# Performance work log

Measured on AMD Instinct MI355X. Metric: run time of the kernel, lower is better.

## Reference

```python
import jax, jax.numpy as jnp
import numpy as np
import math

HIDDEN = 128   # hidden_size (per-head dim) used for 1/sqrt(d) scaling
SPAN = 1024    # attn_span
B, M = 32, 1024
K_LEN = M + SPAN


def _unskew(X, span):
    """X: [B, M, K] -> [B, M, span], out[b,m,l] = X[b, m, m+l].
    Equivalent to the torch pad/view/slice trick (shift row m left by m)."""
    _, Mq, _ = X.shape
    rows = jnp.arange(Mq)[:, None]                 # [M,1]
    cols = rows + jnp.arange(span)[None, :]        # [M,span]
    return X[:, rows, cols]


def _skew(X, pad_value):
    """X: [B, M, L] -> [B, M, M+L], out[b,m,j] = X[b,m,j-m] if 0<=j-m<L else pad.
    Equivalent to the torch pad/view/slice trick (shift row m right by m)."""
    _, Mq, L = X.shape
    m = jnp.arange(Mq)[:, None]                    # [M,1]
    rel = jnp.arange(Mq + L)[None, :] - m          # [M, M+L]
    valid = (rel >= 0) & (rel < L)
    gathered = X[:, m, jnp.clip(rel, 0, L - 1)]    # [B, M, M+L]
    return jnp.where(valid, gathered, pad_value)


def setup_inputs() -> dict:
    key = jax.random.key(0)
    k1, k2, k3, k4 = jax.random.split(key, 4)
    return {
        "query": jax.random.normal(k1, (B, M, HIDDEN), dtype=jnp.float32),
        "key": jax.random.normal(k2, (B, K_LEN, HIDDEN), dtype=jnp.float32),
        "value": jax.random.normal(k3, (B, K_LEN, HIDDEN), dtype=jnp.float32),
        "pos_encoding": jax.random.normal(k4, (HIDDEN, SPAN), dtype=jnp.float32),
    }


def reference(query, key, value, pos_encoding):
    span = pos_encoding.shape[-1]
    # context scores: [B, M, M+span]
    attn_ctx = jnp.einsum('bmh,bkh->bmk', query, key)
    attn_ctx = _unskew(attn_ctx, span)             # [B, M, span]
    # relative-position scores: [B, M, span]
    attn_pos = jnp.einsum('bmh,hl->bml', query, pos_encoding)
    attn = (attn_ctx + attn_pos) / math.sqrt(HIDDEN)
    attn = jax.nn.softmax(attn, axis=-1)           # dropout p=0 -> identity
    attn_sk = _skew(attn, 0.0)                     # [B, M, M+span]
    return jnp.einsum('bmk,bkh->bmh', attn_sk, value)
```

## Files before the change

### kernel.cpp

```cpp
#include <hip/hip_runtime.h>
#include <hip/hip_bf16.h>

#define B_    32
#define M_    1024
#define H_    128
#define SPAN_ 1024
#define KL_   2048
#define NITER 17
#define SCALE 0.08838834764831845f

typedef __attribute__((ext_vector_type(8))) short bf16x8;
typedef __attribute__((ext_vector_type(4))) float f32x4;

#define QOFF 0ull
#define KOFF 8388608ull
#define VOFF 25165824ull
#define POFF 41943040ull
#define WSNEED 42205184ull

static __device__ __forceinline__ unsigned int cvt_pk2(float lo, float hi) {
  unsigned int r;
  asm("v_cvt_pk_bf16_f32 %0, %1, %2" : "=v"(r) : "v"(lo), "v"(hi));
  return r;
}
static __device__ __forceinline__ unsigned short f2b(float x) {
  unsigned int u = __builtin_bit_cast(unsigned int, x);
  return (unsigned short)((u + 0x7FFFu + ((u >> 16) & 1u)) >> 16);
}
static __device__ __forceinline__ float b2f(unsigned short u) {
  return __builtin_bit_cast(float, ((unsigned int)u) << 16);
}
static __device__ __forceinline__ bf16x8 ldfrag(const char* p) {
  short4 a = *(const short4*)p;
  short4 b = *(const short4*)(p + 8);
  bf16x8 r;
  r[0] = a.x; r[1] = a.y; r[2] = a.z; r[3] = a.w;
  r[4] = b.x; r[5] = b.y; r[6] = b.z; r[7] = b.w;
  return r;
}
static __device__ __forceinline__ void gll16(char* lds, const char* g) {
  __builtin_amdgcn_global_load_lds(
      (const __attribute__((address_space(1))) unsigned int*)g,
      (__attribute__((address_space(3))) unsigned int*)lds, 16, 0, 0);
}

__global__ void convA(const float* __restrict__ in, char* __restrict__ out,
                      int nunits, float scale) {
  int idx = blockIdx.x * 256 + threadIdx.x;
  if (idx >= nunits) return;
  int r = idx >> 4, u = idx & 15;
  const float* p = in + (size_t)r * 128 + u * 8;
  float4 a = *(const float4*)p, b = *(const float4*)(p + 4);
  uint4 d;
  d.x = cvt_pk2(a.x * scale, a.y * scale);
  d.y = cvt_pk2(a.z * scale, a.w * scale);
  d.z = cvt_pk2(b.x * scale, b.y * scale);
  d.w = cvt_pk2(b.z * scale, b.w * scale);
  *(uint4*)(out + (size_t)r * 256 + 16 * (u ^ (r & 7))) = d;
}

__global__ void convV(const float* __restrict__ v, char* __restrict__ out) {
  __shared__ float tile[64][130];
  int tb = blockIdx.x;
  const float* src = v + (size_t)tb * 64 * 128;
  int tid = threadIdx.x;
#pragma unroll
  for (int i = 0; i < 8; ++i) {
    int idx = i * 256 + tid;
    int row = idx >> 5, c4 = idx & 31;
    float4 x = *(const float4*)(src + row * 128 + c4 * 4);
    tile[row][c4 * 4 + 0] = x.x; tile[row][c4 * 4 + 1] = x.y;
    tile[row][c4 * 4 + 2] = x.z; tile[row][c4 * 4 + 3] = x.w;
  }
  __syncthreads();
  char* dst = out + (size_t)tb * 16384;
#pragma unroll
  for (int j = 0; j < 4; ++j) {
    int idx = j * 256 + tid;
    int h = idx >> 3, u = idx & 7;
    uint4 d;
    d.x = cvt_pk2(tile[8 * u + 0][h], tile[8 * u + 1][h]);
    d.y = cvt_pk2(tile[8 * u + 2][h], tile[8 * u + 3][h]);
    d.z = cvt_pk2(tile[8 * u + 4][h], tile[8 * u + 5][h]);
    d.w = cvt_pk2(tile[8 * u + 6][h], tile[8 * u + 7][h]);
    *(uint4*)(dst + h * 128 + 16 * (u ^ (h & 7))) = d;
  }
}

__global__ void convP(const float* __restrict__ pe, char* __restrict__ out) {
  __shared__ float tile[128][66];
  int lt = blockIdx.x, tid = threadIdx.x;
#pragma unroll
  for (int i = 0; i < 8; ++i) {
    int idx = i * 256 + tid;
    int h = idx >> 4, c4 = idx & 15;
    float4 x = *(const float4*)(pe + (size_t)h * 1024 + lt * 64 + c4 * 4);
    tile[h][c4 * 4 + 0] = x.x; tile[h][c4 * 4 + 1] = x.y;
    tile[h][c4 * 4 + 2] = x.z; tile[h][c4 * 4 + 3] = x.w;
  }
  __syncthreads();
  char* dst = out + (size_t)lt * 16384;
#pragma unroll
  for (int j = 0; j < 4; ++j) {
    int idx = j * 256 + tid;
    int l = idx >> 4, u = idx & 15;
    uint4 d;
    d.x = cvt_pk2(tile[8 * u + 0][l], tile[8 * u + 1][l]);
    d.y = cvt_pk2(tile[8 * u + 2][l], tile[8 * u + 3][l]);
    d.z = cvt_pk2(tile[8 * u + 4][l], tile[8 * u + 5][l]);
    d.w = cvt_pk2(tile[8 * u + 6][l], tile[8 * u + 7][l]);
    *(uint4*)(dst + l * 256 + 16 * (u ^ (l & 7))) = d;
  }
}

#define L_KL 0
#define L_VT 16384
#define L_PT 32768
#define L_PR 49152
#define L_PW 66048
#define LDS_MAIN 74752

__global__ void __launch_bounds__(256, 2) seqattn_main(
    const char* __restrict__ qws, const char* __restrict__ kws,
    const char* __restrict__ vws, const char* __restrict__ pws,
    float* __restrict__ out) {
  extern __shared__ char smem[];
  char* KL = smem + L_KL;
  char* VT = smem + L_VT;
  char* PT = smem + L_PT;
  char* PR = smem + L_PR;
  char* PW = smem + L_PW;

  int jb = blockIdx.x;
  int o  = (jb & 7) * 64 + (jb >> 3);
  int b  = o >> 4;
  int m0t = o & 15;

  int tid = threadIdx.x, w = tid >> 6, lane = tid & 63, g = lane >> 4, c = lane & 15;
  int mrow = 16 * w + c;
  int sx = c & 7;
  int foffA[4], foffV[2];
#pragma unroll
  for (int hs = 0; hs < 4; ++hs) foffA[hs] = 16 * (((hs << 2) | g) ^ sx);
  foffV[0] = 16 * (g ^ sx);
  foffV[1] = 16 * ((4 | g) ^ sx);

  const char* qsrc = qws + ((size_t)(b * 16 + m0t)) * 16384;
  const char* ksrc = kws + ((size_t)(b * 32 + m0t)) * 16384;
  const char* vsrc = vws + ((size_t)(b * 32 + m0t)) * 16384;

#pragma unroll
  for (int i = 0; i < 4; ++i)
    gll16(KL + (4 * w + i) * 1024, qsrc + (4 * w + i) * 1024 + lane * 16);
  __syncthreads();
  bf16x8 qf[4];
#pragma unroll
  for (int hs = 0; hs < 4; ++hs)
    qf[hs] = *(const bf16x8*)(KL + mrow * 256 + foffA[hs]);
  __syncthreads();
#pragma unroll
  for (int i = 0; i < 4; ++i) {
    gll16(KL + (4 * w + i) * 1024, ksrc + (4 * w + i) * 1024 + lane * 16);
    gll16(VT + (4 * w + i) * 1024, vsrc + (4 * w + i) * 1024 + lane * 16);
    gll16(PT + (4 * w + i) * 1024, pws + (4 * w + i) * 1024 + lane * 16);
  }
  __syncthreads();

  f32x4 O[8];
#pragma unroll
  for (int i = 0; i < 8; ++i) { O[i][0] = 0.f; O[i][1] = 0.f; O[i][2] = 0.f; O[i][3] = 0.f; }
  float mrun = -1e30f, lrun = 0.f;
  char* prRow = PR + mrow * 264;
  char* pwRow = PW + mrow * 136;

#pragma unroll 1
  for (int t = 0; t < NITER; ++t) {
    if (t < 16) {
#pragma unroll
      for (int lt = 0; lt < 4; ++lt) {
        f32x4 pb = {0.f, 0.f, 0.f, 0.f};
#pragma unroll
        for (int hs = 0; hs < 4; ++hs)
          pb = __builtin_amdgcn_mfma_f32_16x16x32_bf16(
              *(const bf16x8*)(PT + (16 * lt + c) * 256 + foffA[hs]), qf[hs], pb, 0, 0, 0);
#pragma unroll
        for (int rr = 0; rr < 4; ++rr) {
          int x = (64 * t + 16 * lt + 4 * g + rr + mrow) & 127;
          *(unsigned short*)(prRow + x * 2) = f2b(pb[rr]);
        }
      }
    }
    f32x4 s[4];
#pragma unroll
    for (int nt = 0; nt < 4; ++nt) {
      f32x4 acc = {0.f, 0.f, 0.f, 0.f};
#pragma unroll
      for (int hs = 0; hs < 4; ++hs)
        acc = __builtin_amdgcn_mfma_f32_16x16x32_bf16(
            *(const bf16x8*)(KL + (16 * nt + c) * 256 + foffA[hs]), qf[hs], acc, 0, 0, 0);
      s[nt] = acc;
    }
    bf16x8 vf[16];
#pragma unroll
    for (int nt = 0; nt < 8; ++nt)
#pragma unroll
      for (int ks = 0; ks < 2; ++ks)
        vf[nt * 2 + ks] = *(const bf16x8*)(VT + (16 * nt + c) * 128 + foffV[ks]);

    __syncthreads();
    if (t < 16) {
      const char* ks_ = ksrc + (size_t)(t + 1) * 16384;
      const char* vs_ = vsrc + (size_t)(t + 1) * 16384;
#pragma unroll
      for (int i = 0; i < 4; ++i) {
        gll16(KL + (4 * w + i) * 1024, ks_ + (4 * w + i) * 1024 + lane * 16);
        gll16(VT + (4 * w + i) * 1024, vs_ + (4 * w + i) * 1024 + lane * 16);
      }
      if (t < 15) {
        const char* ps_ = pws + (size_t)(t + 1) * 16384;
#pragma unroll
        for (int i = 0; i < 4; ++i)
          gll16(PT + (4 * w + i) * 1024, ps_ + (4 * w + i) * 1024 + lane * 16);
      }
    }

#pragma unroll
    for (int nt = 0; nt < 4; ++nt) {
      int x = (64 * t + 16 * nt + 4 * g) & 127;
      ushort4 bv = *(const ushort4*)(prRow + x * 2);
      int lbase = 64 * t + 16 * nt + 4 * g - mrow;
      const unsigned short* bp = (const unsigned short*)&bv;
#pragma unroll
      for (int rr = 0; rr < 4; ++rr) {
        float sv = s[nt][rr] + b2f(bp[rr]);
        s[nt][rr] = ((unsigned)(lbase + rr) < 1024u) ? sv : -1e30f;
      }
    }
    float pmax = -1e30f;
#pragma unroll
    for (int nt = 0; nt < 4; ++nt)
#pragma unroll
      for (int rr = 0; rr < 4; ++rr) pmax = fmaxf(pmax, s[nt][rr]);
    pmax = fmaxf(pmax, __shfl_xor(pmax, 16, 64));
    pmax = fmaxf(pmax, __shfl_xor(pmax, 32, 64));
    if (__any(pmax > mrun + 8.0f)) {
      float mn = fmaxf(mrun, pmax);
      float corr = __expf(mrun - mn);
      mrun = mn;
      lrun *= corr;
#pragma unroll
      for (int i = 0; i < 8; ++i) {
        O[i][0] *= corr; O[i][1] *= corr; O[i][2] *= corr; O[i][3] *= corr;
      }
    }
    float rsum = 0.f;
#pragma unroll
    for (int nt = 0; nt < 4; ++nt) {
      float p0 = __expf(s[nt][0] - mrun);
      float p1 = __expf(s[nt][1] - mrun);
      float p2 = __expf(s[nt][2] - mrun);
      float p3 = __expf(s[nt][3] - mrun);
      rsum += (p0 + p1) + (p2 + p3);
      uint2 d_;
      d_.x = cvt_pk2(p0, p1);
      d_.y = cvt_pk2(p2, p3);
      *(uint2*)(pwRow + (16 * nt + 4 * g) * 2) = d_;
    }
    rsum += __shfl_xor(rsum, 16, 64);
    rsum += __shfl_xor(rsum, 32, 64);
    lrun += rsum;
#pragma unroll
    for (int ks = 0; ks < 2; ++ks) {
      bf16x8 pfrag = ldfrag(pwRow + ks * 64 + g * 16);
#pragma unroll
      for (int nt = 0; nt < 8; ++nt)
        O[nt] = __builtin_amdgcn_mfma_f32_16x16x32_bf16(
            vf[nt * 2 + ks], pfrag, O[nt], 0, 0, 0);
    }
    __syncthreads();
  }

  float inv = 1.0f / lrun;
  float* ob = out + ((size_t)b * M_ + m0t * 64 + mrow) * H_;
#pragma unroll
  for (int nt = 0; nt < 8; ++nt) {
    float4 vv;
    vv.x = O[nt][0] * inv; vv.y = O[nt][1] * inv;
    vv.z = O[nt][2] * inv; vv.w = O[nt][3] * inv;
    *(float4*)(ob + 16 * nt + 4 * g) = vv;
  }
}

#define PITCH_A  264
#define PITCH_VT 136
#define PITCH_PR 264
#define PITCH_PW 136
#define OFF_K  0
#define OFF_VT 16896
#define OFF_PT 34304
#define OFF_PR 51200
#define OFF_PW 68096
#define LDS_FB 76800

__global__ void __launch_bounds__(256, 2) seqattn_fb(
    const float* __restrict__ q, const float* __restrict__ kkey,
    const float* __restrict__ vval, const float* __restrict__ pe,
    float* __restrict__ out) {
  extern __shared__ char smem[];
  char* KL = smem + OFF_K;
  char* VT = smem + OFF_VT;
  char* PT = smem + OFF_PT;
  char* PR = smem + OFF_PR;
  char* PW = smem + OFF_PW;

  int jb = blockIdx.x;
  int o  = (jb & 7) * 64 + (jb >> 3);
  int b  = o >> 4;
  int m0 = (o & 15) * 64;

  int tid  = threadIdx.x;
  int w    = tid >> 6;
  int lane = tid & 63;
  int g    = lane >> 4;
  int c    = lane & 15;
  int r0   = tid >> 5;
  int c4   = tid & 31;

  const float* qbase = q    + ((size_t)b * M_  + m0) * H_;
  const float* kbase = kkey + ((size_t)b * KL_ + m0) * H_;
  const float* vbase = vval + ((size_t)b * KL_ + m0) * H_;

  float4 kpre[8];
  float  vpre[32];
  float  ppre[32];

#define LOADK(tt) do {                                                        \
    const float* kb_ = kbase + (size_t)(64 * (tt)) * H_;                      \
    _Pragma("unroll")                                                         \
    for (int p = 0; p < 8; ++p)                                               \
      kpre[p] = *(const float4*)(kb_ + (p * 8 + r0) * H_ + c4 * 4);           \
  } while (0)
#define WRITEK() do {                                                         \
    _Pragma("unroll")                                                         \
    for (int p = 0; p < 8; ++p) {                                             \
      float4 v_ = kpre[p];                                                    \
      uint2 d_; d_.x = cvt_pk2(v_.x, v_.y); d_.y = cvt_pk2(v_.z, v_.w);       \
      *(uint2*)(KL + (p * 8 + r0) * PITCH_A + c4 * 8) = d_;                   \
    }                                                                         \
  } while (0)
#define LOADV(tt) do {                                                        \
    const float* vb_ = vbase + (size_t)(64 * (tt)) * H_;                      \
    _Pragma("unroll")                                                         \
    for (int qq = 0; qq < 4; ++qq) {                                          \
      int kq_ = 4 * (4 * w + qq);                                             \
      _Pragma("unroll")                                                       \
      for (int r = 0; r < 4; ++r) {                                           \
        vpre[qq * 8 + r * 2 + 0] = vb_[(kq_ + r) * H_ + lane];                \
        vpre[qq * 8 + r * 2 + 1] = vb_[(kq_ + r) * H_ + lane + 64];           \
      }                                                                       \
    }                                                                         \
  } while (0)
#define WRITEV() do {                                                         \
    _Pragma("unroll")                                                         \
    for (int qq = 0; qq < 4; ++qq) {                                          \
      int kq_ = 4 * w + qq;                                                   \
      uint2 lo_, hi_;                                                         \
      lo_.x = cvt_pk2(vpre[qq * 8 + 0], vpre[qq * 8 + 2]);                    \
      lo_.y = cvt_pk2(vpre[qq * 8 + 4], vpre[qq * 8 + 6]);                    \
      hi_.x = cvt_pk2(vpre[qq * 8 + 1], vpre[qq * 8 + 3]);                    \
      hi_.y = cvt_pk2(vpre[qq * 8 + 5], vpre[qq * 8 + 7]);                    \
      *(uint2*)(VT + lane * PITCH_VT + 8 * kq_) = lo_;                        \
      *(uint2*)(VT + (lane + 64) * PITCH_VT + 8 * kq_) = hi_;                 \
    }                                                                         \
  } while (0)
#define LOADP(tt) do {                                                        \
    const float* pb_ = pe + 64 * (tt);                                        \
    _Pragma("unroll")                                                         \
    for (int qq = 0; qq < 8; ++qq) {                                          \
      int h_ = 4 * (8 * w + qq);                                              \
      _Pragma("unroll")                                                       \
      for (int r = 0; r < 4; ++r)                                             \
        ppre[qq * 4 + r] = pb_[(h_ + r) * SPAN_ + lane];                      \
    }                                                                         \
  } while (0)
#define WRITEP() do {                                                         \
    _Pragma("unroll")                                                         \
    for (int qq = 0; qq < 8; ++qq) {                                          \
      uint2 d_;                                                               \
      d_.x = cvt_pk2(ppre[qq * 4 + 0], ppre[qq * 4 + 1]);                     \
      d_.y = cvt_pk2(ppre[qq * 4 + 2], ppre[qq * 4 + 3]);                     \
      *(uint2*)(PT + lane * PITCH_A + 8 * (8 * w + qq)) = d_;                 \
    }                                                                         \
  } while (0)

  {
    float4 qpre[8];
#pragma unroll
    for (int p = 0; p < 8; ++p)
      qpre[p] = *(const float4*)(qbase + (p * 8 + r0) * H_ + c4 * 4);
    LOADK(0); LOADV(0); LOADP(0);
#pragma unroll
    for (int p = 0; p < 8; ++p) {
      float4 v_ = qpre[p];
      uint2 d_;
      d_.x = cvt_pk2(v_.x * SCALE, v_.y * SCALE);
      d_.y = cvt_pk2(v_.z * SCALE, v_.w * SCALE);
      *(uint2*)(PR + (p * 8 + r0) * PITCH_PR + c4 * 8) = d_;
    }
    WRITEK(); WRITEV(); WRITEP();
    LOADK(1); LOADV(1); LOADP(1);
  }
  __syncthreads();

  bf16x8 qf[4];
#pragma unroll
  for (int hs = 0; hs < 4; ++hs)
    qf[hs] = ldfrag(PR + (w * 16 + c) * PITCH_PR + hs * 64 + g * 16);

  f32x4 O[8];
#pragma unroll
  for (int i = 0; i < 8; ++i) { O[i][0] = 0.f; O[i][1] = 0.f; O[i][2] = 0.f; O[i][3] = 0.f; }
  float mrun = -1e30f, lrun = 0.f;
  const int mrow = 16 * w + c;
  char* prRow = PR + mrow * PITCH_PR;
  char* pwRow = PW + mrow * PITCH_PW;

#pragma unroll 1
  for (int t = 0; t < NITER; ++t) {
    if (t < 16) {
#pragma unroll
      for (int lt = 0; lt < 4; ++lt) {
        f32x4 pb = {0.f, 0.f, 0.f, 0.f};
#pragma unroll
        for (int hs = 0; hs < 4; ++hs)
          pb = __builtin_amdgcn_mfma_f32_16x16x32_bf16(
              ldfrag(PT + (16 * lt + c) * PITCH_A + hs * 64 + g * 16), qf[hs], pb, 0, 0, 0);
#pragma unroll
        for (int rr = 0; rr < 4; ++rr) {
          int x = (64 * t + 16 * lt + 4 * g + rr + mrow) & 127;
          *(unsigned short*)(prRow + x * 2) = f2b(pb[rr]);
        }
      }
    }
    f32x4 s[4];
#pragma unroll
    for (int nt = 0; nt < 4; ++nt) {
      f32x4 acc = {0.f, 0.f, 0.f, 0.f};
#pragma unroll
      for (int hs = 0; hs < 4; ++hs)
        acc = __builtin_amdgcn_mfma_f32_16x16x32_bf16(
            ldfrag(KL + (16 * nt + c) * PITCH_A + hs * 64 + g * 16), qf[hs], acc, 0, 0, 0);
      s[nt] = acc;
    }
#pragma unroll
    for (int nt = 0; nt < 4; ++nt) {
      int x = (64 * t + 16 * nt + 4 * g) & 127;
      ushort4 bv = *(const ushort4*)(prRow + x * 2);
      int lbase = 64 * t + 16 * nt + 4 * g - mrow;
      const unsigned short* bp = (const unsigned short*)&bv;
#pragma unroll
      for (int rr = 0; rr < 4; ++rr) {
        float sv = s[nt][rr] + b2f(bp[rr]);
        s[nt][rr] = ((unsigned)(lbase + rr) < 1024u) ? sv : -1e30f;
      }
    }
    float pmax = -1e30f;
#pragma unroll
    for (int nt = 0; nt < 4; ++nt)
#pragma unroll
      for (int rr = 0; rr < 4; ++rr) pmax = fmaxf(pmax, s[nt][rr]);
    pmax = fmaxf(pmax, __shfl_xor(pmax, 16, 64));
    pmax = fmaxf(pmax, __shfl_xor(pmax, 32, 64));
    if (__any(pmax > mrun + 8.0f)) {
      float mn = fmaxf(mrun, pmax);
      float corr = __expf(mrun - mn);
      mrun = mn;
      lrun *= corr;
#pragma unroll
      for (int i = 0; i < 8; ++i) {
        O[i][0] *= corr; O[i][1] *= corr; O[i][2] *= corr; O[i][3] *= corr;
      }
    }
    float rsum = 0.f;
#pragma unroll
    for (int nt = 0; nt < 4; ++nt) {
      float p0 = __expf(s[nt][0] - mrun);
      float p1 = __expf(s[nt][1] - mrun);
      float p2 = __expf(s[nt][2] - mrun);
      float p3 = __expf(s[nt][3] - mrun);
      rsum += (p0 + p1) + (p2 + p3);
      uint2 d_;
      d_.x = cvt_pk2(p0, p1);
      d_.y = cvt_pk2(p2, p3);
      *(uint2*)(pwRow + (16 * nt + 4 * g) * 2) = d_;
    }
    rsum += __shfl_xor(rsum, 16, 64);
    rsum += __shfl_xor(rsum, 32, 64);
    lrun += rsum;
#pragma unroll
    for (int ks = 0; ks < 2; ++ks) {
      bf16x8 pfrag = ldfrag(pwRow + ks * 64 + g * 16);
#pragma unroll
      for (int nt = 0; nt < 8; ++nt)
        O[nt] = __builtin_amdgcn_mfma_f32_16x16x32_bf16(
            ldfrag(VT + (16 * nt + c) * PITCH_VT + ks * 64 + g * 16), pfrag, O[nt], 0, 0, 0);
    }
    __syncthreads();
    if (t < 16) {
      WRITEK(); WRITEV();
      if (t < 15) {
        WRITEP();
        LOADK(t + 2); LOADV(t + 2);
        if (t + 2 < 16) LOADP(t + 2);
      }
    }
    __syncthreads();
  }

  float inv = 1.0f / lrun;
  float* ob = out + ((size_t)b * M_ + m0 + mrow) * H_;
#pragma unroll
  for (int nt = 0; nt < 8; ++nt) {
    float4 vv;
    vv.x = O[nt][0] * inv; vv.y = O[nt][1] * inv;
    vv.z = O[nt][2] * inv; vv.w = O[nt][3] * inv;
    *(float4*)(ob + 16 * nt + 4 * g) = vv;
  }
}
#undef LOADK
#undef WRITEK
#undef LOADV
#undef WRITEV
#undef LOADP
#undef WRITEP

extern "C" void kernel_launch(void* const* d_in, const int* in_sizes, int n_in,
                              void* d_out, int out_size, void* d_ws, size_t ws_size,
                              hipStream_t stream) {
  const float* q  = (const float*)d_in[0];
  const float* k  = (const float*)d_in[1];
  const float* v  = (const float*)d_in[2];
  const float* pe = (const float*)d_in[3];
  float* out = (float*)d_out;

  if (ws_size >= WSNEED) {
    char* ws = (char*)d_ws;
    convA<<<dim3(2048), dim3(256), 0, stream>>>(q, ws + QOFF, 32 * 1024 * 16, SCALE);
    convA<<<dim3(4096), dim3(256), 0, stream>>>(k, ws + KOFF, 32 * 2048 * 16, 1.0f);
    convV<<<dim3(1024), dim3(256), 0, stream>>>(v, ws + VOFF);
    convP<<<dim3(16), dim3(256), 0, stream>>>(pe, ws + POFF);
    hipFuncSetAttribute(reinterpret_cast<const void*>(seqattn_main),
                        hipFuncAttributeMaxDynamicSharedMemorySize, LDS_MAIN);
    seqattn_main<<<dim3(512), dim3(256), LDS_MAIN, stream>>>(
        ws + QOFF, ws + KOFF, ws + VOFF, ws + POFF, out);
  } else {
    hipFuncSetAttribute(reinterpret_cast<const void*>(seqattn_fb),
                        hipFuncAttributeMaxDynamicSharedMemorySize, LDS_FB);
    seqattn_fb<<<dim3(512), dim3(256), LDS_FB, stream>>>(q, k, v, pe, out);
  }
}
```

Before: 88.43 us.

## Double query tile per block with double-buffered K/V and fused conversion kernel

Merges the four bf16 conversion kernels into one launch. The main attention kernel now processes 128 query rows per block (two 16-row fragments per wave), so each K, V and positional-encoding fragment loaded from LDS feeds two MFMAs. K/V tiles are double-buffered so the next tile's load overlaps compute, and the positional-bias ring grows to 192 entries. The block count halves to 256 and LDS rises to about 146 KB with one block per CU, which reduces occupancy and latency hiding.

Measured after the change: 103.7 us. 17.2% more time.

```diff
diff --git a/kernel.cpp b/kernel.cpp
--- a/kernel.cpp
+++ b/kernel.cpp
@@ -6,7 +6,6 @@
 #define H_    128
 #define SPAN_ 1024
 #define KL_   2048
-#define NITER 17
 #define SCALE 0.08838834764831845f
 
 typedef __attribute__((ext_vector_type(8))) short bf16x8;
@@ -44,100 +43,110 @@
       (__attribute__((address_space(3))) unsigned int*)lds, 16, 0, 0);
 }
 
-__global__ void convA(const float* __restrict__ in, char* __restrict__ out,
-                      int nunits, float scale) {
-  int idx = blockIdx.x * 256 + threadIdx.x;
-  if (idx >= nunits) return;
-  int r = idx >> 4, u = idx & 15;
-  const float* p = in + (size_t)r * 128 + u * 8;
-  float4 a = *(const float4*)p, b = *(const float4*)(p + 4);
-  uint4 d;
-  d.x = cvt_pk2(a.x * scale, a.y * scale);
-  d.y = cvt_pk2(a.z * scale, a.w * scale);
-  d.z = cvt_pk2(b.x * scale, b.y * scale);
-  d.w = cvt_pk2(b.z * scale, b.w * scale);
-  *(uint4*)(out + (size_t)r * 256 + 16 * (u ^ (r & 7))) = d;
-}
-
-__global__ void convV(const float* __restrict__ v, char* __restrict__ out) {
-  __shared__ float tile[64][130];
-  int tb = blockIdx.x;
-  const float* src = v + (size_t)tb * 64 * 128;
-  int tid = threadIdx.x;
-#pragma unroll
-  for (int i = 0; i < 8; ++i) {
-    int idx = i * 256 + tid;
-    int row = idx >> 5, c4 = idx & 31;
-    float4 x = *(const float4*)(src + row * 128 + c4 * 4);
-    tile[row][c4 * 4 + 0] = x.x; tile[row][c4 * 4 + 1] = x.y;
-    tile[row][c4 * 4 + 2] = x.z; tile[row][c4 * 4 + 3] = x.w;
-  }
-  __syncthreads();
-  char* dst = out + (size_t)tb * 16384;
-#pragma unroll
-  for (int j = 0; j < 4; ++j) {
-    int idx = j * 256 + tid;
-    int h = idx >> 3, u = idx & 7;
+__global__ void __launch_bounds__(256) convAll(
+    const float* __restrict__ q, const float* __restrict__ k,
+    const float* __restrict__ v, const float* __restrict__ pe,
+    char* __restrict__ ws) {
+  __shared__ float tile[8448];
+  int bid = blockIdx.x, tid = threadIdx.x;
+  if (bid < 6144) {
+    const float* in;
+    char* out;
+    float scale;
+    int base;
+    if (bid < 2048) { in = q; out = ws + QOFF; scale = SCALE; base = bid; }
+    else            { in = k; out = ws + KOFF; scale = 1.0f;  base = bid - 2048; }
+    int idx = base * 256 + tid;
+    int r = idx >> 4, u = idx & 15;
+    const float* p = in + (size_t)r * 128 + u * 8;
+    float4 a = *(const float4*)p, b = *(const float4*)(p + 4);
     uint4 d;
-    d.x = cvt_pk2(tile[8 * u + 0][h], tile[8 * u + 1][h]);
-    d.y = cvt_pk2(tile[8 * u + 2][h], tile[8 * u + 3][h]);
-    d.z = cvt_pk2(tile[8 * u + 4][h], tile[8 * u + 5][h]);
-    d.w = cvt_pk2(tile[8 * u + 6][h], tile[8 * u + 7][h]);
-    *(uint4*)(dst + h * 128 + 16 * (u ^ (h & 7))) = d;
-  }
-}
-
-__global__ void convP(const float* __restrict__ pe, char* __restrict__ out) {
-  __shared__ float tile[128][66];
-  int lt = blockIdx.x, tid = threadIdx.x;
-#pragma unroll
-  for (int i = 0; i < 8; ++i) {
-    int idx = i * 256 + tid;
-    int h = idx >> 4, c4 = idx & 15;
-    float4 x = *(const float4*)(pe + (size_t)h * 1024 + lt * 64 + c4 * 4);
-    tile[h][c4 * 4 + 0] = x.x; tile[h][c4 * 4 + 1] = x.y;
-    tile[h][c4 * 4 + 2] = x.z; tile[h][c4 * 4 + 3] = x.w;
-  }
-  __syncthreads();
-  char* dst = out + (size_t)lt * 16384;
-#pragma unroll
-  for (int j = 0; j < 4; ++j) {
-    int idx = j * 256 + tid;
-    int l = idx >> 4, u = idx & 15;
-    uint4 d;
-    d.x = cvt_pk2(tile[8 * u + 0][l], tile[8 * u + 1][l]);
-    d.y = cvt_pk2(tile[8 * u + 2][l], tile[8 * u + 3][l]);
-    d.z = cvt_pk2(tile[8 * u + 4][l], tile[8 * u + 5][l]);
-    d.w = cvt_pk2(tile[8 * u + 6][l], tile[8 * u + 7][l]);
-    *(uint4*)(dst + l * 256 + 16 * (u ^ (l & 7))) = d;
-  }
-}
-
-#define L_KL 0
-#define L_VT 16384
-#define L_PT 32768
-#define L_PR 49152
-#define L_PW 66048
-#define LDS_MAIN 74752
-
-__global__ void __launch_bounds__(256, 2) seqattn_main(
+    d.x = cvt_pk2(a.x * scale, a.y * scale);
+    d.y = cvt_pk2(a.z * scale, a.w * scale);
+    d.z = cvt_pk2(b.x * scale, b.y * scale);
+    d.w = cvt_pk2(b.z * scale, b.w * scale);
+    *(uint4*)(out + (size_t)r * 256 + 16 * (u ^ (r & 7))) = d;
+  } else if (bid < 7168) {
+    int tb = bid - 6144;
+    const float* src = v + (size_t)tb * 64 * 128;
+#pragma unroll
+    for (int i = 0; i < 8; ++i) {
+      int idx = i * 256 + tid;
+      int row = idx >> 5, c4 = idx & 31;
+      float4 x = *(const float4*)(src + row * 128 + c4 * 4);
+      tile[row * 130 + c4 * 4 + 0] = x.x; tile[row * 130 + c4 * 4 + 1] = x.y;
+      tile[row * 130 + c4 * 4 + 2] = x.z; tile[row * 130 + c4 * 4 + 3] = x.w;
+    }
+    __syncthreads();
+    char* dst = ws + VOFF + (size_t)tb * 16384;
+#pragma unroll
+    for (int j = 0; j < 2; ++j) {
+      int idx = j * 256 + tid;
+      int h = idx & 127;
+      int u0 = idx >> 7;
+#pragma unroll
+      for (int uu = 0; uu < 2; ++uu) {
+        int u = u0 * 2 + uu;
+        uint4 d;
+        d.x = cvt_pk2(tile[(8 * u + 0) * 130 + h], tile[(8 * u + 1) * 130 + h]);
+        d.y = cvt_pk2(tile[(8 * u + 2) * 130 + h], tile[(8 * u + 3) * 130 + h]);
+        d.z = cvt_pk2(tile[(8 * u + 4) * 130 + h], tile[(8 * u + 5) * 130 + h]);
+        d.w = cvt_pk2(tile[(8 * u + 6) * 130 + h], tile[(8 * u + 7) * 130 + h]);
+        *(uint4*)(dst + h * 128 + 16 * (u ^ (h & 7))) = d;
+      }
+    }
+  } else {
+    int lt = bid - 7168;
+#pragma unroll
+    for (int i = 0; i < 8; ++i) {
+      int idx = i * 256 + tid;
+      int h = idx >> 4, c4 = idx & 15;
+      float4 x = *(const float4*)(pe + (size_t)h * 1024 + lt * 64 + c4 * 4);
+      tile[h * 66 + c4 * 4 + 0] = x.x; tile[h * 66 + c4 * 4 + 1] = x.y;
+      tile[h * 66 + c4 * 4 + 2] = x.z; tile[h * 66 + c4 * 4 + 3] = x.w;
+    }
+    __syncthreads();
+    char* dst = ws + POFF + (size_t)lt * 16384;
+#pragma unroll
+    for (int j = 0; j < 4; ++j) {
+      int u = tid >> 4;
+      int l = (tid & 15) + 16 * j;
+      uint4 d;
+      d.x = cvt_pk2(tile[(8 * u + 0) * 66 + l], tile[(8 * u + 1) * 66 + l]);
+      d.y = cvt_pk2(tile[(8 * u + 2) * 66 + l], tile[(8 * u + 3) * 66 + l]);
+      d.z = cvt_pk2(tile[(8 * u + 4) * 66 + l], tile[(8 * u + 5) * 66 + l]);
+      d.w = cvt_pk2(tile[(8 * u + 6) * 66 + l], tile[(8 * u + 7) * 66 + l]);
+      *(uint4*)(dst + l * 256 + 16 * (u ^ (l & 7))) = d;
+    }
+  }
+}
+
+#define L_KL0 0
+#define L_VT0 16384
+#define L_KL1 32768
+#define L_VT1 49152
+#define L_PT  65536
+#define L_PR  81920
+#define L_PW  132096
+#define LDS_MAIN 149504
+#define NIT2 18
+
+__global__ void __launch_bounds__(256, 1) seqattn_main(
     const char* __restrict__ qws, const char* __restrict__ kws,
     const char* __restrict__ vws, const char* __restrict__ pws,
     float* __restrict__ out) {
   extern __shared__ char smem[];
-  char* KL = smem + L_KL;
-  char* VT = smem + L_VT;
   char* PT = smem + L_PT;
   char* PR = smem + L_PR;
   char* PW = smem + L_PW;
+  char* QSTG = smem + L_KL1;
 
   int jb = blockIdx.x;
-  int o  = (jb & 7) * 64 + (jb >> 3);
-  int b  = o >> 4;
-  int m0t = o & 15;
+  int o  = (jb & 7) * 32 + (jb >> 3);
+  int b  = o >> 3;
+  int mt = o & 7;
 
   int tid = threadIdx.x, w = tid >> 6, lane = tid & 63, g = lane >> 4, c = lane & 15;
-  int mrow = 16 * w + c;
   int sx = c & 7;
   int foffA[4], foffV[2];
 #pragma unroll
@@ -145,76 +154,90 @@
   foffV[0] = 16 * (g ^ sx);
   foffV[1] = 16 * ((4 | g) ^ sx);
 
-  const char* qsrc = qws + ((size_t)(b * 16 + m0t)) * 16384;
-  const char* ksrc = kws + ((size_t)(b * 32 + m0t)) * 16384;
-  const char* vsrc = vws + ((size_t)(b * 32 + m0t)) * 16384;
-
-#pragma unroll
-  for (int i = 0; i < 4; ++i)
-    gll16(KL + (4 * w + i) * 1024, qsrc + (4 * w + i) * 1024 + lane * 16);
+  const char* qsrc = qws + (size_t)(b * 16 + mt * 2) * 16384;
+  const char* ksrc = kws + (size_t)(b * 32 + mt * 2) * 16384;
+  const char* vsrc = vws + (size_t)(b * 32 + mt * 2) * 16384;
+
+#pragma unroll
+  for (int i = 0; i < 8; ++i) {
+    int cq = 8 * w + i;
+    gll16(QSTG + cq * 1024, qsrc + cq * 1024 + lane * 16);
+  }
+#pragma unroll
+  for (int i = 0; i < 4; ++i) {
+    gll16(smem + L_KL0 + (4 * w + i) * 1024, ksrc + (4 * w + i) * 1024 + lane * 16);
+    gll16(smem + L_VT0 + (4 * w + i) * 1024, vsrc + (4 * w + i) * 1024 + lane * 16);
+    gll16(PT + (4 * w + i) * 1024, pws + (4 * w + i) * 1024 + lane * 16);
+  }
   __syncthreads();
-  bf16x8 qf[4];
-#pragma unroll
-  for (int hs = 0; hs < 4; ++hs)
-    qf[hs] = *(const bf16x8*)(KL + mrow * 256 + foffA[hs]);
+
+  int rowq[2] = {32 * w + c, 32 * w + 16 + c};
+  bf16x8 qf[2][4];
+#pragma unroll
+  for (int qh = 0; qh < 2; ++qh)
+#pragma unroll
+    for (int hs = 0; hs < 4; ++hs)
+      qf[qh][hs] = *(const bf16x8*)(QSTG + rowq[qh] * 256 + foffA[hs]);
   __syncthreads();
-#pragma unroll
-  for (int i = 0; i < 4; ++i) {
-    gll16(KL + (4 * w + i) * 1024, ksrc + (4 * w + i) * 1024 + lane * 16);
-    gll16(VT + (4 * w + i) * 1024, vsrc + (4 * w + i) * 1024 + lane * 16);
-    gll16(PT + (4 * w + i) * 1024, pws + (4 * w + i) * 1024 + lane * 16);
-  }
-  __syncthreads();
-
-  f32x4 O[8];
-#pragma unroll
-  for (int i = 0; i < 8; ++i) { O[i][0] = 0.f; O[i][1] = 0.f; O[i][2] = 0.f; O[i][3] = 0.f; }
-  float mrun = -1e30f, lrun = 0.f;
-  char* prRow = PR + mrow * 264;
-  char* pwRow = PW + mrow * 136;
+
+  f32x4 O[2][8];
+#pragma unroll
+  for (int qh = 0; qh < 2; ++qh)
+#pragma unroll
+    for (int i = 0; i < 8; ++i) {
+      O[qh][i][0] = 0.f; O[qh][i][1] = 0.f; O[qh][i][2] = 0.f; O[qh][i][3] = 0.f;
+    }
+  float mrun[2] = {-1e30f, -1e30f}, lrun[2] = {0.f, 0.f};
+  char* prRow[2];
+  char* pwRow[2];
+#pragma unroll
+  for (int qh = 0; qh < 2; ++qh) {
+    prRow[qh] = PR + rowq[qh] * 392;
+    pwRow[qh] = PW + rowq[qh] * 136;
+  }
+  int ringbase = 0;
 
 #pragma unroll 1
-  for (int t = 0; t < NITER; ++t) {
+  for (int t = 0; t < NIT2; ++t) {
+    char* KL = smem + ((t & 1) ? L_KL1 : L_KL0);
+    char* VT = smem + ((t & 1) ? L_VT1 : L_VT0);
+
     if (t < 16) {
 #pragma unroll
       for (int lt = 0; lt < 4; ++lt) {
-        f32x4 pb = {0.f, 0.f, 0.f, 0.f};
-#pragma unroll
-        for (int hs = 0; hs < 4; ++hs)
-          pb = __builtin_amdgcn_mfma_f32_16x16x32_bf16(
-              *(const bf16x8*)(PT + (16 * lt + c) * 256 + foffA[hs]), qf[hs], pb, 0, 0, 0);
-#pragma unroll
-        for (int rr = 0; rr < 4; ++rr) {
-          int x = (64 * t + 16 * lt + 4 * g + rr + mrow) & 127;
-          *(unsigned short*)(prRow + x * 2) = f2b(pb[rr]);
+        f32x4 pb[2];
+#pragma unroll
+        for (int qh = 0; qh < 2; ++qh) {
+          pb[qh][0] = 0.f; pb[qh][1] = 0.f; pb[qh][2] = 0.f; pb[qh][3] = 0.f;
         }
-      }
-    }
-    f32x4 s[4];
-#pragma unroll
-    for (int nt = 0; nt < 4; ++nt) {
-      f32x4 acc = {0.f, 0.f, 0.f, 0.f};
-#pragma unroll
-      for (int hs = 0; hs < 4; ++hs)
-        acc = __builtin_amdgcn_mfma_f32_16x16x32_bf16(
-            *(const bf16x8*)(KL + (16 * nt + c) * 256 + foffA[hs]), qf[hs], acc, 0, 0, 0);
-      s[nt] = acc;
-    }
-    bf16x8 vf[16];
-#pragma unroll
-    for (int nt = 0; nt < 8; ++nt)
-#pragma unroll
-      for (int ks = 0; ks < 2; ++ks)
-        vf[nt * 2 + ks] = *(const bf16x8*)(VT + (16 * nt + c) * 128 + foffV[ks]);
-
+#pragma unroll
+        for (int hs = 0; hs < 4; ++hs) {
+          bf16x8 pf = *(const bf16x8*)(PT + (16 * lt + c) * 256 + foffA[hs]);
+#pragma unroll
+          for (int qh = 0; qh < 2; ++qh)
+            pb[qh] = __builtin_amdgcn_mfma_f32_16x16x32_bf16(pf, qf[qh][hs], pb[qh], 0, 0, 0);
+        }
+#pragma unroll
+        for (int qh = 0; qh < 2; ++qh)
+#pragma unroll
+          for (int rr = 0; rr < 4; ++rr) {
+            int x = ringbase + 16 * lt + 4 * g + rr + rowq[qh];
+            x = (x >= 192) ? x - 192 : x;
+            *(unsigned short*)(prRow[qh] + x * 2) = f2b(pb[qh][rr]);
+          }
+      }
+    }
     __syncthreads();
-    if (t < 16) {
+
+    if (t < NIT2 - 1) {
       const char* ks_ = ksrc + (size_t)(t + 1) * 16384;
       const char* vs_ = vsrc + (size_t)(t + 1) * 16384;
+      char* KLn = smem + ((t & 1) ? L_KL0 : L_KL1);
+      char* VTn = smem + ((t & 1) ? L_VT0 : L_VT1);
 #pragma unroll
       for (int i = 0; i < 4; ++i) {
-        gll16(KL + (4 * w + i) * 1024, ks_ + (4 * w + i) * 1024 + lane * 16);
-        gll16(VT + (4 * w + i) * 1024, vs_ + (4 * w + i) * 1024 + lane * 16);
+        gll16(KLn + (4 * w + i) * 1024, ks_ + (4 * w + i) * 1024 + lane * 16);
+        gll16(VTn + (4 * w + i) * 1024, vs_ + (4 * w + i) * 1024 + lane * 16);
       }
       if (t < 15) {
         const char* ps_ = pws + (size_t)(t + 1) * 16384;
@@ -224,70 +247,103 @@
       }
     }
 
+    f32x4 s[2][4];
 #pragma unroll
     for (int nt = 0; nt < 4; ++nt) {
-      int x = (64 * t + 16 * nt + 4 * g) & 127;
-      ushort4 bv = *(const ushort4*)(prRow + x * 2);
-      int lbase = 64 * t + 16 * nt + 4 * g - mrow;
-      const unsigned short* bp = (const unsigned short*)&bv;
-#pragma unroll
-      for (int rr = 0; rr < 4; ++rr) {
-        float sv = s[nt][rr] + b2f(bp[rr]);
-        s[nt][rr] = ((unsigned)(lbase + rr) < 1024u) ? sv : -1e30f;
-      }
-    }
-    float pmax = -1e30f;
-#pragma unroll
-    for (int nt = 0; nt < 4; ++nt)
-#pragma unroll
-      for (int rr = 0; rr < 4; ++rr) pmax = fmaxf(pmax, s[nt][rr]);
-    pmax = fmaxf(pmax, __shfl_xor(pmax, 16, 64));
-    pmax = fmaxf(pmax, __shfl_xor(pmax, 32, 64));
-    if (__any(pmax > mrun + 8.0f)) {
-      float mn = fmaxf(mrun, pmax);
-      float corr = __expf(mrun - mn);
-      mrun = mn;
-      lrun *= corr;
-#pragma unroll
-      for (int i = 0; i < 8; ++i) {
-        O[i][0] *= corr; O[i][1] *= corr; O[i][2] *= corr; O[i][3] *= corr;
-      }
-    }
-    float rsum = 0.f;
-#pragma unroll
-    for (int nt = 0; nt < 4; ++nt) {
-      float p0 = __expf(s[nt][0] - mrun);
-      float p1 = __expf(s[nt][1] - mrun);
-      float p2 = __expf(s[nt][2] - mrun);
-      float p3 = __expf(s[nt][3] - mrun);
-      rsum += (p0 + p1) + (p2 + p3);
-      uint2 d_;
-      d_.x = cvt_pk2(p0, p1);
-      d_.y = cvt_pk2(p2, p3);
-      *(uint2*)(pwRow + (16 * nt + 4 * g) * 2) = d_;
-    }
-    rsum += __shfl_xor(rsum, 16, 64);
-    rsum += __shfl_xor(rsum, 32, 64);
-    lrun += rsum;
+      f32x4 a[2];
+#pragma unroll
+      for (int qh = 0; qh < 2; ++qh) {
+        a[qh][0] = 0.f; a[qh][1] = 0.f; a[qh][2] = 0.f; a[qh][3] = 0.f;
+      }
+#pragma unroll
+      for (int hs = 0; hs < 4; ++hs) {
+        bf16x8 kf = *(const bf16x8*)(KL + (16 * nt + c) * 256 + foffA[hs]);
+#pragma unroll
+        for (int qh = 0; qh < 2; ++qh)
+          a[qh] = __builtin_amdgcn_mfma_f32_16x16x32_bf16(kf, qf[qh][hs], a[qh], 0, 0, 0);
+      }
+#pragma unroll
+      for (int qh = 0; qh < 2; ++qh) s[qh][nt] = a[qh];
+    }
+
+#pragma unroll
+    for (int qh = 0; qh < 2; ++qh) {
+      float pmax = -1e30f;
+#pragma unroll
+      for (int nt = 0; nt < 4; ++nt) {
+        int x = ringbase + 16 * nt + 4 * g;
+        ushort4 bv = *(const ushort4*)(prRow[qh] + x * 2);
+        int lbase = 64 * t + 16 * nt + 4 * g - rowq[qh];
+        const unsigned short* bp = (const unsigned short*)&bv;
+#pragma unroll
+        for (int rr = 0; rr < 4; ++rr) {
+          float sv = s[qh][nt][rr] + b2f(bp[rr]);
+          sv = ((unsigned)(lbase + rr) < 1024u) ? sv : -1e30f;
+          s[qh][nt][rr] = sv;
+          pmax = fmaxf(pmax, sv);
+        }
+      }
+      pmax = fmaxf(pmax, __shfl_xor(pmax, 16, 64));
+      pmax = fmaxf(pmax, __shfl_xor(pmax, 32, 64));
+      if (__any(pmax > mrun[qh] + 8.0f)) {
+        float mn = fmaxf(mrun[qh], pmax);
+        float corr = __expf(mrun[qh] - mn);
+        mrun[qh] = mn;
+        lrun[qh] *= corr;
+#pragma unroll
+        for (int i = 0; i < 8; ++i) {
+          O[qh][i][0] *= corr; O[qh][i][1] *= corr;
+          O[qh][i][2] *= corr; O[qh][i][3] *= corr;
+        }
+      }
+      float rsum = 0.f;
+#pragma unroll
+      for (int nt = 0; nt < 4; ++nt) {
+        float p0 = __expf(s[qh][nt][0] - mrun[qh]);
+        float p1 = __expf(s[qh][nt][1] - mrun[qh]);
+        float p2 = __expf(s[qh][nt][2] - mrun[qh]);
+        float p3 = __expf(s[qh][nt][3] - mrun[qh]);
+        rsum += (p0 + p1) + (p2 + p3);
+        uint2 d_;
+        d_.x = cvt_pk2(p0, p1);
+        d_.y = cvt_pk2(p2, p3);
+        *(uint2*)(pwRow[qh] + (16 * nt + 4 * g) * 2) = d_;
+      }
+      rsum += __shfl_xor(rsum, 16, 64);
+      rsum += __shfl_xor(rsum, 32, 64);
+      lrun[qh] += rsum;
+    }
+
 #pragma unroll
     for (int ks = 0; ks < 2; ++ks) {
-      bf16x8 pfrag = ldfrag(pwRow + ks * 64 + g * 16);
-#pragma unroll
-      for (int nt = 0; nt < 8; ++nt)
-        O[nt] = __builtin_amdgcn_mfma_f32_16x16x32_bf16(
-            vf[nt * 2 + ks], pfrag, O[nt], 0, 0, 0);
+      bf16x8 pf2[2];
+#pragma unroll
+      for (int qh = 0; qh < 2; ++qh)
+        pf2[qh] = ldfrag(pwRow[qh] + ks * 64 + g * 16);
+#pragma unroll
+      for (int nt = 0; nt < 8; ++nt) {
+        bf16x8 vfr = *(const bf16x8*)(VT + (16 * nt + c) * 128 + foffV[ks]);
+#pragma unroll
+        for (int qh = 0; qh < 2; ++qh)
+          O[qh][nt] = __builtin_amdgcn_mfma_f32_16x16x32_bf16(vfr, pf2[qh], O[qh][nt], 0, 0, 0);
+      }
     }
     __syncthreads();
-  }
-
-  float inv = 1.0f / lrun;
-  float* ob = out + ((size_t)b * M_ + m0t * 64 + mrow) * H_;
-#pragma unroll
-  for (int nt = 0; nt < 8; ++nt) {
-    float4 vv;
-    vv.x = O[nt][0] * inv; vv.y = O[nt][1] * inv;
-    vv.z = O[nt][2] * inv; vv.w = O[nt][3] * inv;
-    *(float4*)(ob + 16 * nt + 4 * g) = vv;
+    ringbase += 64;
+    if (ringbase >= 192) ringbase -= 192;
+  }
+
+#pragma unroll
+  for (int qh = 0; qh < 2; ++qh) {
+    float inv = 1.0f / lrun[qh];
+    float* ob = out + ((size_t)b * M_ + mt * 128 + rowq[qh]) * H_;
+#pragma unroll
+    for (int nt = 0; nt < 8; ++nt) {
+      float4 vv;
+      vv.x = O[qh][nt][0] * inv; vv.y = O[qh][nt][1] * inv;
+      vv.z = O[qh][nt][2] * inv; vv.w = O[qh][nt][3] * inv;
+      *(float4*)(ob + 16 * nt + 4 * g) = vv;
+    }
   }
 }
 
@@ -301,6 +357,7 @@
 #define OFF_PR 51200
 #define OFF_PW 68096
 #define LDS_FB 76800
+#define NITER 17
 
 __global__ void __launch_bounds__(256, 2) seqattn_fb(
     const float* __restrict__ q, const float* __restrict__ kkey,
@@ -545,17 +602,14 @@
 
   if (ws_size >= WSNEED) {
     char* ws = (char*)d_ws;
-    convA<<<dim3(2048), dim3(256), 0, stream>>>(q, ws + QOFF, 32 * 1024 * 16, SCALE);
-    convA<<<dim3(4096), dim3(256), 0, stream>>>(k, ws + KOFF, 32 * 2048 * 16, 1.0f);
-    convV<<<dim3(1024), dim3(256), 0, stream>>>(v, ws + VOFF);
-    convP<<<dim3(16), dim3(256), 0, stream>>>(pe, ws + POFF);
-    hipFuncSetAttribute(reinterpret_cast<const void*>(seqattn_main),
-                        hipFuncAttributeMaxDynamicSharedMemorySize, LDS_MAIN);
-    seqattn_main<<<dim3(512), dim3(256), LDS_MAIN, stream>>>(
+    convAll<<<dim3(7184), dim3(256), 0, stream>>>(q, k, v, pe, ws);
+    (void)hipFuncSetAttribute(reinterpret_cast<const void*>(seqattn_main),
+                              hipFuncAttributeMaxDynamicSharedMemorySize, LDS_MAIN);
+    seqattn_main<<<dim3(256), dim3(256), LDS_MAIN, stream>>>(
         ws + QOFF, ws + KOFF, ws + VOFF, ws + POFF, out);
   } else {
-    hipFuncSetAttribute(reinterpret_cast<const void*>(seqattn_fb),
-                        hipFuncAttributeMaxDynamicSharedMemorySize, LDS_FB);
+    (void)hipFuncSetAttribute(reinterpret_cast<const void*>(seqattn_fb),
+                              hipFuncAttributeMaxDynamicSharedMemorySize, LDS_FB);
     seqattn_fb<<<dim3(512), dim3(256), LDS_FB, stream>>>(q, k, v, pe, out);
   }
 }
```
